# Kernel tuning notes

Hardware: AMD Instinct MI355X
Metric: run time of the kernel (lower is better)

Reference implementation:

```python
import jax, jax.numpy as jnp
import numpy as np

N_NODES = 100000
N_EDGES = 1600000


def _leaky_relu(x, slope=0.1):
    return jnp.where(x > 0, x, slope * x)


def _sage_conv(x, src, dst, Wl, Wr, b, n_nodes):
    # mean aggregation of source messages onto target nodes (PyG SAGEConv, aggr='mean')
    msg = x[src]                                              # [E, d] gather
    agg_sum = jax.ops.segment_sum(msg, dst, num_segments=n_nodes)
    cnt = jax.ops.segment_sum(jnp.ones((src.shape[0],), x.dtype), dst, num_segments=n_nodes)
    agg = agg_sum / jnp.maximum(cnt, 1.0)[:, None]            # empty neighborhoods -> 0
    # out = lin_l(agg) + lin_r(x); bias lives in lin_l
    return agg @ Wl + x @ Wr + b


def setup_inputs() -> dict:
    key = jax.random.key(0)
    ks = jax.random.split(key, 8)
    x = jax.random.normal(ks[0], (N_NODES, 128), dtype=jnp.float32)
    edge_index = jax.random.randint(ks[1], (2, N_EDGES), 0, N_NODES, dtype=jnp.int32)
    scale = 0.05
    Wl_stack = jax.random.normal(ks[2], (3, 128, 128), dtype=jnp.float32) * scale
    Wr_stack = jax.random.normal(ks[3], (3, 128, 128), dtype=jnp.float32) * scale
    b_stack = jax.random.normal(ks[4], (3, 128), dtype=jnp.float32) * scale
    Wl_out = jax.random.normal(ks[5], (128, 64), dtype=jnp.float32) * scale
    Wr_out = jax.random.normal(ks[6], (128, 64), dtype=jnp.float32) * scale
    b_out = jax.random.normal(ks[7], (64,), dtype=jnp.float32) * scale
    return {"x": x, "edge_index": edge_index, "Wl_stack": Wl_stack,
            "Wr_stack": Wr_stack, "b_stack": b_stack,
            "Wl_out": Wl_out, "Wr_out": Wr_out, "b_out": b_out}


def reference(x, edge_index, Wl_stack, Wr_stack, b_stack, Wl_out, Wr_out, b_out):
    src, dst = edge_index[0], edge_index[1]
    n = x.shape[0]
    h = x
    # conv1 + hidden convs, each followed by LeakyReLU(0.1)
    for i in range(Wl_stack.shape[0]):
        h = _leaky_relu(_sage_conv(h, src, dst, Wl_stack[i], Wr_stack[i], b_stack[i], n))
    # final SAGEConv without activation
    out = _sage_conv(h, src, dst, Wl_out, Wr_out, b_out, n)
    return out
```

## Files before the change

### kernel.cpp

```cpp
#include <hip/hip_runtime.h>

#define NN 100000
#define NNP 100096
#define NE 1600000
#define NBK 391
#define SCCH 4096
#define NSC ((NE + SCCH - 1) / SCCH)

typedef __attribute__((ext_vector_type(8))) short bf16x8;
typedef __attribute__((ext_vector_type(4))) float f32x4;

__device__ __forceinline__ float bf2f(unsigned short u) {
    unsigned int v = ((unsigned int)u) << 16;
    return __builtin_bit_cast(float, v);
}
__device__ __forceinline__ unsigned short f2bf(float f) {
    unsigned int u = __builtin_bit_cast(unsigned int, f);
    u += 0x7FFFu + ((u >> 16) & 1u);
    return (unsigned short)(u >> 16);
}
__device__ __forceinline__ unsigned int pk2(float lo, float hi) {
    return (unsigned int)f2bf(lo) | ((unsigned int)f2bf(hi) << 16);
}
__device__ __forceinline__ float bflo(unsigned int v) {
    return __builtin_bit_cast(float, v << 16);
}
__device__ __forceinline__ float bfhi(unsigned int v) {
    return __builtin_bit_cast(float, v & 0xFFFF0000u);
}


__global__ __launch_bounds__(256) void kb_hist(const int* __restrict__ dst,
                                               int* __restrict__ bcnt) {
    __shared__ int lh[NBK];
    int tid = threadIdx.x;
    for (int i = tid; i < NBK; i += 256) lh[i] = 0;
    __syncthreads();
    int base = blockIdx.x * SCCH;
    int lim = min(SCCH, NE - base);
    for (int i = tid; i < lim; i += 256)
        atomicAdd(&lh[dst[base + i] >> 8], 1);
    __syncthreads();
    for (int i = tid; i < NBK; i += 256)
        if (lh[i]) atomicAdd(&bcnt[i], lh[i]);
}

__global__ __launch_bounds__(512) void kb_scan(const int* __restrict__ bcnt,
                                               int* __restrict__ boff,
                                               int* __restrict__ bcur) {
    __shared__ int s[512];
    int tid = threadIdx.x;
    int v = (tid < NBK) ? bcnt[tid] : 0;
    s[tid] = v;
    __syncthreads();
#pragma unroll
    for (int off = 1; off < 512; off <<= 1) {
        int t = (tid >= off) ? s[tid - off] : 0;
        __syncthreads();
        if (tid >= off) s[tid] += t;
        __syncthreads();
    }
    if (tid < NBK) {
        int e = s[tid] - v;
        boff[tid] = e;
        bcur[tid] = e;
    }
    if (tid == 0) boff[NBK] = NE;
}

__global__ __launch_bounds__(256) void kb_scatter(const int* __restrict__ src,
                                                  const int* __restrict__ dst,
                                                  int* __restrict__ bcur,
                                                  unsigned long long* __restrict__ ebuf) {
    __shared__ int lh[NBK], lbase[NBK];
    int tid = threadIdx.x;
    for (int i = tid; i < NBK; i += 256) lh[i] = 0;
    __syncthreads();
    int base = blockIdx.x * SCCH;
    int lim = min(SCCH, NE - base);
    for (int i = tid; i < lim; i += 256)
        atomicAdd(&lh[dst[base + i] >> 8], 1);
    __syncthreads();
    for (int i = tid; i < NBK; i += 256)
        lbase[i] = lh[i] ? atomicAdd(&bcur[i], lh[i]) : 0;
    __syncthreads();
    for (int i = tid; i < NBK; i += 256) lh[i] = 0;
    __syncthreads();
    for (int i = tid; i < lim; i += 256) {
        int d = dst[base + i];
        int s = src[base + i];
        int b = d >> 8;
        int off = atomicAdd(&lh[b], 1);
        ebuf[(size_t)lbase[b] + off] =
            ((unsigned long long)(unsigned)d << 32) | (unsigned)s;
    }
}

__global__ __launch_bounds__(256) void kb_csr(const unsigned long long* __restrict__ ebuf,
                                              const int* __restrict__ boff,
                                              int* __restrict__ row_off,
                                              int* __restrict__ csr) {
    __shared__ int sdeg[256], spre[256];
    int bkt = blockIdx.x;
    int tid = threadIdx.x;
    int nbase = bkt << 8;
    int ebeg = boff[bkt], eend = boff[bkt + 1];
    sdeg[tid] = 0;
    __syncthreads();
    for (int e = ebeg + tid; e < eend; e += 256) {
        int d = (int)(ebuf[e] >> 32);
        atomicAdd(&sdeg[d & 255], 1);
    }
    __syncthreads();
    spre[tid] = sdeg[tid];
    __syncthreads();
#pragma unroll
    for (int off = 1; off < 256; off <<= 1) {
        int t = (tid >= off) ? spre[tid - off] : 0;
        __syncthreads();
        if (tid >= off) spre[tid] += t;
        __syncthreads();
    }
    int excl = spre[tid] - sdeg[tid];
    if (nbase + tid < NN) row_off[nbase + tid] = ebeg + excl;
    if (bkt == 0 && tid == 0) row_off[NN] = NE;
    __syncthreads();
    sdeg[tid] = excl;
    __syncthreads();
    for (int e = ebeg + tid; e < eend; e += 256) {
        unsigned long long pv = ebuf[e];
        int d = (int)(pv >> 32);
        int s = (int)(unsigned)pv;
        int p = atomicAdd(&sdeg[d & 255], 1);
        csr[ebeg + p] = s;
    }
}


__global__ __launch_bounds__(256) void k_prep_wt(const float* __restrict__ Wl_stack,
                                                 const float* __restrict__ Wr_stack,
                                                 const float* __restrict__ Wl_out,
                                                 const float* __restrict__ Wr_out,
                                                 unsigned short* __restrict__ WT) {
    int i = blockIdx.x * 256 + threadIdx.x;
    const int L3OFF = 3 * 256 * 128;
    const int TOT = L3OFF + 128 * 128;
    if (i >= TOT) return;
    float v;
    if (i < L3OFF) {
        int l = i / (256 * 128);
        int r = i % (256 * 128);
        int c = r / 128;
        int k = r % 128;
        v = (c < 128) ? Wl_stack[(size_t)(l * 128 + k) * 128 + c]
                      : Wr_stack[(size_t)(l * 128 + k) * 128 + (c - 128)];
    } else {
        int r = i - L3OFF;
        int c = r / 128;
        int k = r % 128;
        v = (c < 64) ? Wl_out[(size_t)k * 64 + c]
                     : Wr_out[(size_t)k * 64 + (c - 64)];
    }
    WT[i] = f2bf(v);
}


template <int NOUT, bool F32IN>
__global__ __launch_bounds__(256) void k_mm(const void* __restrict__ Ain,
                                            const unsigned short* __restrict__ WT,
                                            unsigned short* __restrict__ Y,
                                            unsigned short* __restrict__ Z) {
    constexpr int S = (NOUT == 128) ? 4 : 2;
    int tid = threadIdx.x;
    int wave = tid >> 6, l = tid & 63;
    int lrow = l & 15, g = l >> 4;
    int rbase, cbase;
    if (NOUT == 128) {
        rbase = blockIdx.x * 128 + (wave & 1) * 64;
        cbase = (wave >> 1) * 128;
    } else {
        rbase = blockIdx.x * 128 + wave * 32;
        cbase = 0;
    }

    bf16x8 af[S][4];
#pragma unroll
    for (int s = 0; s < S; ++s) {
        int row = rbase + s * 16 + lrow;
#pragma unroll
        for (int ks = 0; ks < 4; ++ks) {
            if (F32IN) {
                int rc = row < NN ? row : NN - 1;
                const float* ap = (const float*)Ain + (size_t)rc * 128 + ks * 32 + g * 8;
                float4 a = *(const float4*)ap;
                float4 b = *(const float4*)(ap + 4);
                uint4 u;
                u.x = pk2(a.x, a.y); u.y = pk2(a.z, a.w);
                u.z = pk2(b.x, b.y); u.w = pk2(b.z, b.w);
                af[s][ks] = __builtin_bit_cast(bf16x8, u);
            } else {
                af[s][ks] = *(const bf16x8*)((const unsigned short*)Ain
                                             + (size_t)row * 128 + ks * 32 + g * 8);
            }
        }
    }

#pragma unroll
    for (int cg = 0; cg < 8; ++cg) {
        int c0 = cbase + cg * 16;
        bf16x8 bfr[4];
#pragma unroll
        for (int ks = 0; ks < 4; ++ks)
            bfr[ks] = *(const bf16x8*)(WT + (size_t)(c0 + lrow) * 128 + ks * 32 + g * 8);
        unsigned short* dstp = (c0 < NOUT) ? Y : Z;
        int cb = ((c0 < NOUT) ? c0 : c0 - NOUT) + g * 4;
#pragma unroll
        for (int s = 0; s < S; ++s) {
            f32x4 acc = {0.f, 0.f, 0.f, 0.f};
#pragma unroll
            for (int ks = 0; ks < 4; ++ks)
                acc = __builtin_amdgcn_mfma_f32_16x16x32_bf16(bfr[ks], af[s][ks], acc, 0, 0, 0);
            int row = rbase + s * 16 + lrow;
            uint2 w;
            w.x = pk2(acc[0], acc[1]);
            w.y = pk2(acc[2], acc[3]);
            *(uint2*)(dstp + (size_t)row * NOUT + cb) = w;
        }
    }
}


template <int NOUT, bool RELU>
__global__ __launch_bounds__(256) void k_aggb(const unsigned short* __restrict__ Y,
                                              const unsigned short* __restrict__ Z,
                                              const int* __restrict__ row_off,
                                              const int* __restrict__ csr,
                                              const float* __restrict__ b,
                                              unsigned short* __restrict__ outb,
                                              float* __restrict__ outf) {
    int lane = threadIdx.x & 63;
    int n = __builtin_amdgcn_readfirstlane(blockIdx.x * 4 + (threadIdx.x >> 6));
    if (n >= NN) return;
    int beg = __builtin_amdgcn_readfirstlane(row_off[n]);
    int end = __builtin_amdgcn_readfirstlane(row_off[n + 1]);
    float inv = (end > beg) ? 1.0f / (float)(end - beg) : 0.0f;

    if (NOUT == 128) {
        const int lane2 = lane * 2;
        float a0 = 0.f, a1 = 0.f;
        int e = beg;
        for (; e + 8 <= end; e += 8) {
            int s0 = csr[e + 0], s1 = csr[e + 1], s2 = csr[e + 2], s3 = csr[e + 3];
            int s4 = csr[e + 4], s5 = csr[e + 5], s6 = csr[e + 6], s7 = csr[e + 7];
            unsigned int v0 = *(const unsigned int*)(Y + (size_t)s0 * 128 + lane2);
            unsigned int v1 = *(const unsigned int*)(Y + (size_t)s1 * 128 + lane2);
            unsigned int v2 = *(const unsigned int*)(Y + (size_t)s2 * 128 + lane2);
            unsigned int v3 = *(const unsigned int*)(Y + (size_t)s3 * 128 + lane2);
            unsigned int v4 = *(const unsigned int*)(Y + (size_t)s4 * 128 + lane2);
            unsigned int v5 = *(const unsigned int*)(Y + (size_t)s5 * 128 + lane2);
            unsigned int v6 = *(const unsigned int*)(Y + (size_t)s6 * 128 + lane2);
            unsigned int v7 = *(const unsigned int*)(Y + (size_t)s7 * 128 + lane2);
            a0 += bflo(v0) + bflo(v1) + bflo(v2) + bflo(v3)
                + bflo(v4) + bflo(v5) + bflo(v6) + bflo(v7);
            a1 += bfhi(v0) + bfhi(v1) + bfhi(v2) + bfhi(v3)
                + bfhi(v4) + bfhi(v5) + bfhi(v6) + bfhi(v7);
        }
        for (; e + 4 <= end; e += 4) {
            int s0 = csr[e + 0], s1 = csr[e + 1], s2 = csr[e + 2], s3 = csr[e + 3];
            unsigned int v0 = *(const unsigned int*)(Y + (size_t)s0 * 128 + lane2);
            unsigned int v1 = *(const unsigned int*)(Y + (size_t)s1 * 128 + lane2);
            unsigned int v2 = *(const unsigned int*)(Y + (size_t)s2 * 128 + lane2);
            unsigned int v3 = *(const unsigned int*)(Y + (size_t)s3 * 128 + lane2);
            a0 += bflo(v0) + bflo(v1) + bflo(v2) + bflo(v3);
            a1 += bfhi(v0) + bfhi(v1) + bfhi(v2) + bfhi(v3);
        }
        for (; e < end; ++e) {
            int s = csr[e];
            unsigned int v = *(const unsigned int*)(Y + (size_t)s * 128 + lane2);
            a0 += bflo(v);
            a1 += bfhi(v);
        }
        unsigned int zv = *(const unsigned int*)(Z + (size_t)n * 128 + lane2);
        float2 bb = *(const float2*)(b + lane2);
        float o0 = a0 * inv + bflo(zv) + bb.x;
        float o1 = a1 * inv + bfhi(zv) + bb.y;
        if (RELU) {
            o0 = o0 > 0.f ? o0 : 0.1f * o0;
            o1 = o1 > 0.f ? o1 : 0.1f * o1;
        }
        *(unsigned int*)(outb + (size_t)n * 128 + lane2) = pk2(o0, o1);
    } else {
        float a0 = 0.f;
        int e = beg;
        for (; e + 8 <= end; e += 8) {
            int s0 = csr[e + 0], s1 = csr[e + 1], s2 = csr[e + 2], s3 = csr[e + 3];
            int s4 = csr[e + 4], s5 = csr[e + 5], s6 = csr[e + 6], s7 = csr[e + 7];
            float f0 = bf2f(Y[(size_t)s0 * 64 + lane]);
            float f1 = bf2f(Y[(size_t)s1 * 64 + lane]);
            float f2 = bf2f(Y[(size_t)s2 * 64 + lane]);
            float f3 = bf2f(Y[(size_t)s3 * 64 + lane]);
            float f4 = bf2f(Y[(size_t)s4 * 64 + lane]);
            float f5 = bf2f(Y[(size_t)s5 * 64 + lane]);
            float f6 = bf2f(Y[(size_t)s6 * 64 + lane]);
            float f7 = bf2f(Y[(size_t)s7 * 64 + lane]);
            a0 += f0 + f1 + f2 + f3 + f4 + f5 + f6 + f7;
        }
        for (; e + 4 <= end; e += 4) {
            int s0 = csr[e + 0], s1 = csr[e + 1], s2 = csr[e + 2], s3 = csr[e + 3];
            float f0 = bf2f(Y[(size_t)s0 * 64 + lane]);
            float f1 = bf2f(Y[(size_t)s1 * 64 + lane]);
            float f2 = bf2f(Y[(size_t)s2 * 64 + lane]);
            float f3 = bf2f(Y[(size_t)s3 * 64 + lane]);
            a0 += f0 + f1 + f2 + f3;
        }
        for (; e < end; ++e) {
            int s = csr[e];
            a0 += bf2f(Y[(size_t)s * 64 + lane]);
        }
        float o = a0 * inv + bf2f(Z[(size_t)n * 64 + lane]) + b[lane];
        if (RELU) o = o > 0.f ? o : 0.1f * o;
        outf[(size_t)n * 64 + lane] = o;
    }
}


extern "C" void kernel_launch(void* const* d_in, const int* in_sizes, int n_in,
                              void* d_out, int out_size, void* d_ws, size_t ws_size,
                              hipStream_t stream) {
    const float* x        = (const float*)d_in[0];
    const int*   ei       = (const int*)d_in[1];
    const float* Wl_stack = (const float*)d_in[2];
    const float* Wr_stack = (const float*)d_in[3];
    const float* b_stack  = (const float*)d_in[4];
    const float* Wl_out   = (const float*)d_in[5];
    const float* Wr_out   = (const float*)d_in[6];
    const float* b_out    = (const float*)d_in[7];
    float* out = (float*)d_out;

    unsigned short* hb = (unsigned short*)d_ws;
    unsigned short* Yb = hb + (size_t)NNP * 128;
    unsigned short* Zb = Yb + (size_t)NNP * 128;
    unsigned short* WT = Zb + (size_t)NNP * 128;
    unsigned long long* ebuf = (unsigned long long*)(WT + 114688);
    int* row_off = (int*)(ebuf + NE);
    int* csr     = row_off + NN + 1;
    int* bcnt    = csr + NE;
    int* boff    = bcnt + NBK;
    int* bcur    = boff + NBK + 1;

    const int* src = ei;
    const int* dst = ei + NE;

    (void)hipMemsetAsync(bcnt, 0, NBK * sizeof(int), stream);
    kb_hist<<<NSC, 256, 0, stream>>>(dst, bcnt);
    kb_scan<<<1, 512, 0, stream>>>(bcnt, boff, bcur);
    kb_scatter<<<NSC, 256, 0, stream>>>(src, dst, bcur, ebuf);
    kb_csr<<<NBK, 256, 0, stream>>>(ebuf, boff, row_off, csr);

    k_prep_wt<<<448, 256, 0, stream>>>(Wl_stack, Wr_stack, Wl_out, Wr_out, WT);

    k_mm<128, true><<<NNP / 128, 256, 0, stream>>>(x, WT, Yb, Zb);
    k_aggb<128, true><<<(NN + 3) / 4, 256, 0, stream>>>(Yb, Zb, row_off, csr,
                                                        b_stack, hb, nullptr);
    for (int l = 1; l < 3; ++l) {
        k_mm<128, false><<<NNP / 128, 256, 0, stream>>>(hb, WT + l * 32768, Yb, Zb);
        k_aggb<128, true><<<(NN + 3) / 4, 256, 0, stream>>>(Yb, Zb, row_off, csr,
                                                            b_stack + l * 128, hb, nullptr);
    }
    k_mm<64, false><<<NNP / 128, 256, 0, stream>>>(hb, WT + 98304, Yb, Zb);
    k_aggb<64, false><<<(NN + 3) / 4, 256, 0, stream>>>(Yb, Zb, row_off, csr,
                                                        b_out, nullptr, out);
}
```

Before: 418.7 us.

## Stage GEMM weights in swizzled LDS and retile blocks to 256 rows

The node-feature GEMM kernel now copies the weight half it needs into an XOR-swizzled 32 KB LDS buffer once per block. Previously every wave fetched its weight fragments straight from global memory. The tiling also changes: each block covers 256 rows, each wave handles 64 rows, and for the 128-wide layers the block index selects which half of the output columns it computes. The launch grids are adjusted to match. This trades global and L2 weight traffic for an LDS fill and a barrier per block, and the LDS footprint may reduce occupancy.

Result: faster. 398.8 us (-4.8%).

```diff
diff --git a/kernel.cpp b/kernel.cpp
--- a/kernel.cpp
+++ b/kernel.cpp
@@ -170,22 +170,31 @@
                                             const unsigned short* __restrict__ WT,
                                             unsigned short* __restrict__ Y,
                                             unsigned short* __restrict__ Z) {
-    constexpr int S = (NOUT == 128) ? 4 : 2;
+    constexpr int HALVES = NOUT / 64;
+    __shared__ unsigned char lds[32768];
+
     int tid = threadIdx.x;
     int wave = tid >> 6, l = tid & 63;
     int lrow = l & 15, g = l >> 4;
-    int rbase, cbase;
-    if (NOUT == 128) {
-        rbase = blockIdx.x * 128 + (wave & 1) * 64;
-        cbase = (wave >> 1) * 128;
-    } else {
-        rbase = blockIdx.x * 128 + wave * 32;
-        cbase = 0;
-    }
-
-    bf16x8 af[S][4];
-#pragma unroll
-    for (int s = 0; s < S; ++s) {
+    int half = (HALVES == 2) ? (blockIdx.x & 1) : 0;
+    int rowblk = (HALVES == 2) ? (blockIdx.x >> 1) : blockIdx.x;
+    int rbase = rowblk * 256 + wave * 64;
+
+    {
+        const unsigned char* wsrc = (const unsigned char*)(WT + (size_t)half * 128 * 128);
+#pragma unroll
+        for (int j = 0; j < 8; ++j) {
+            int lin = (j * 256 + tid) * 16;
+            uint4 v = *(const uint4*)(wsrc + lin);
+            int row = lin >> 8;
+            int colb = lin & 255;
+            *(uint4*)(lds + row * 256 + (colb ^ ((row & 7) << 4))) = v;
+        }
+    }
+
+    bf16x8 af[4][4];
+#pragma unroll
+    for (int s = 0; s < 4; ++s) {
         int row = rbase + s * 16 + lrow;
 #pragma unroll
         for (int ks = 0; ks < 4; ++ks) {
@@ -204,18 +213,23 @@
             }
         }
     }
+    __syncthreads();
 
 #pragma unroll
     for (int cg = 0; cg < 8; ++cg) {
-        int c0 = cbase + cg * 16;
+        int c0 = cg * 16;
+        int rl = c0 + lrow;
         bf16x8 bfr[4];
 #pragma unroll
-        for (int ks = 0; ks < 4; ++ks)
-            bfr[ks] = *(const bf16x8*)(WT + (size_t)(c0 + lrow) * 128 + ks * 32 + g * 8);
-        unsigned short* dstp = (c0 < NOUT) ? Y : Z;
-        int cb = ((c0 < NOUT) ? c0 : c0 - NOUT) + g * 4;
-#pragma unroll
-        for (int s = 0; s < S; ++s) {
+        for (int ks = 0; ks < 4; ++ks) {
+            int colb = ks * 64 + g * 16;
+            bfr[ks] = *(const bf16x8*)(lds + rl * 256 + (colb ^ ((rl & 7) << 4)));
+        }
+        int gc0 = half * 128 + c0;
+        unsigned short* dstp = (gc0 < NOUT) ? Y : Z;
+        int cb = ((gc0 < NOUT) ? gc0 : gc0 - NOUT) + g * 4;
+#pragma unroll
+        for (int s = 0; s < 4; ++s) {
             f32x4 acc = {0.f, 0.f, 0.f, 0.f};
 #pragma unroll
             for (int ks = 0; ks < 4; ++ks)
@@ -359,15 +373,15 @@
 
     k_prep_wt<<<448, 256, 0, stream>>>(Wl_stack, Wr_stack, Wl_out, Wr_out, WT);
 
-    k_mm<128, true><<<NNP / 128, 256, 0, stream>>>(x, WT, Yb, Zb);
+    k_mm<128, true><<<(NNP / 256) * 2, 256, 0, stream>>>(x, WT, Yb, Zb);
     k_aggb<128, true><<<(NN + 3) / 4, 256, 0, stream>>>(Yb, Zb, row_off, csr,
                                                         b_stack, hb, nullptr);
     for (int l = 1; l < 3; ++l) {
-        k_mm<128, false><<<NNP / 128, 256, 0, stream>>>(hb, WT + l * 32768, Yb, Zb);
+        k_mm<128, false><<<(NNP / 256) * 2, 256, 0, stream>>>(hb, WT + l * 32768, Yb, Zb);
         k_aggb<128, true><<<(NN + 3) / 4, 256, 0, stream>>>(Yb, Zb, row_off, csr,
                                                             b_stack + l * 128, hb, nullptr);
     }
-    k_mm<64, false><<<NNP / 128, 256, 0, stream>>>(hb, WT + 98304, Yb, Zb);
+    k_mm<64, false><<<NNP / 256, 256, 0, stream>>>(hb, WT + 98304, Yb, Zb);
     k_aggb<64, false><<<(NN + 3) / 4, 256, 0, stream>>>(Yb, Zb, row_off, csr,
                                                         b_out, nullptr, out);
 }
```
